# Kernel optimization log

Measured on AMD Instinct MI355X. Metric: run time of the kernel, lower is better.

Reference implementation:

```python
import jax, jax.numpy as jnp
import numpy as np

EMB_SIZE = 768
BLOCK_SIZE = 64
NUM_CLASS = 97
N = 4096
NUM_BLOCKS = EMB_SIZE // BLOCK_SIZE  # 12


def setup_inputs() -> dict:
    key = jax.random.key(0)
    k1, k2, k3 = jax.random.split(key, 3)
    head_embeddings = jax.random.normal(k1, (N, EMB_SIZE), dtype=jnp.float32)
    tail_embeddings = jax.random.normal(k2, (N, EMB_SIZE), dtype=jnp.float32)
    # xavier_uniform for [NUM_CLASS, EMB_SIZE*BLOCK_SIZE]
    fan_in = EMB_SIZE * BLOCK_SIZE
    fan_out = NUM_CLASS
    bound = float(np.sqrt(6.0 / (fan_in + fan_out)))
    W = jax.random.uniform(k3, (NUM_CLASS, EMB_SIZE * BLOCK_SIZE), dtype=jnp.float32,
                           minval=-bound, maxval=bound)
    b = jnp.full((NUM_CLASS,), 0.1, dtype=jnp.float32)
    return {"head_embeddings": head_embeddings, "tail_embeddings": tail_embeddings,
            "W": W, "b": b}


def reference(head_embeddings, tail_embeddings, W, b):
    n = head_embeddings.shape[0]
    b1 = head_embeddings.reshape(n, NUM_BLOCKS, BLOCK_SIZE)  # [N, K, S]
    b2 = tail_embeddings.reshape(n, NUM_BLOCKS, BLOCK_SIZE)  # [N, K, S]
    # block-wise outer product: [N, K, S, S] -> [N, K*S*S]
    bl = jnp.einsum('nki,nkj->nkij', b1, b2).reshape(n, EMB_SIZE * BLOCK_SIZE)
    logits = bl @ W.T + b  # [N, NUM_CLASS]
    return logits
```

## Files before the change

### kernel.cpp

```cpp
#include <hip/hip_runtime.h>
#include <hip/hip_bf16.h>
#include <stdint.h>

#define NROWS 4096
#define NCLS  97
#define EMB   768
#define KTOT  49152
#define OUT_ELEMS (NROWS * NCLS)
#define E_ELEMS  (NROWS * EMB)
#define NK32  (KTOT / 32)
#define WT_BYTES ((size_t)NK32 * 128 * 64)
#define EB_BYTES ((size_t)E_ELEMS * 2)

typedef __attribute__((ext_vector_type(8)))  short short8;
typedef __attribute__((ext_vector_type(4)))  float floatx4;
typedef __bf16 bf16x2 __attribute__((ext_vector_type(2)));
typedef __bf16 bf16x8 __attribute__((ext_vector_type(8)));

__device__ __forceinline__ uint32_t pkmul(uint32_t a, uint32_t b) {
  bf16x2 x = __builtin_bit_cast(bf16x2, a);
  bf16x2 y = __builtin_bit_cast(bf16x2, b);
  bf16x2 r = x * y;
  return __builtin_bit_cast(uint32_t, r);
}

__device__ __forceinline__ uint4 cvt8(float4 a, float4 b) {
  bf16x8 v;
  v[0] = (__bf16)a.x; v[1] = (__bf16)a.y; v[2] = (__bf16)a.z; v[3] = (__bf16)a.w;
  v[4] = (__bf16)b.x; v[5] = (__bf16)b.y; v[6] = (__bf16)b.z; v[7] = (__bf16)b.w;
  return __builtin_bit_cast(uint4, v);
}

__global__ void prep(const float* __restrict__ W,
                     const float* __restrict__ b1,
                     const float* __restrict__ b2,
                     uint4* __restrict__ wt,
                     uint4* __restrict__ b1b,
                     uint4* __restrict__ b2b,
                     int nmax)
{
  const int nwt = NK32 * 128 * 4;
  const int nE8 = E_ELEMS / 8;
  int t = blockIdx.x * blockDim.x + threadIdx.x;
  if (t >= nmax) return;
  if (t < nwt) {
    int eo = t & 3;
    int c  = (t >> 2) & 127;
    int kc = t >> 9;
    uint4 v = uint4{0u, 0u, 0u, 0u};
    if (c < NCLS) {
      const float4* p = (const float4*)(W + (size_t)c * KTOT + kc * 32 + eo * 8);
      v = cvt8(p[0], p[1]);
    }
    wt[t] = v;
  } else if (t < nwt + nE8) {
    int i = t - nwt;
    const float4* p = (const float4*)b1 + (size_t)2 * i;
    b1b[i] = cvt8(p[0], p[1]);
  } else {
    int i = t - nwt - nE8;
    const float4* p = (const float4*)b2 + (size_t)2 * i;
    b2b[i] = cvt8(p[0], p[1]);
  }
}

template<bool BMIR>
__global__ __launch_bounds__(256, 2)
void bilinear_main(const void* __restrict__ b1p,
                   const void* __restrict__ b2p,
                   const char* __restrict__ Wt,
                   const float* __restrict__ biasg,
                   float* __restrict__ P,
                   float* __restrict__ outd,
                   int klen)
{
  const int tid  = threadIdx.x;
  const int w    = tid >> 6;
  const int l    = tid & 63;
  const int l15  = l & 15;
  const int quad = l >> 4;
  const int mhalf = w & 1;
  const int chalf = w >> 1;
  const int bm = blockIdx.y;
  const int k0 = blockIdx.x * klen;

  int nrow[4];
#pragma unroll
  for (int rt = 0; rt < 4; ++rt) nrow[rt] = bm * 128 + mhalf * 64 + rt * 16 + l15;

  const char* wtl = Wt + (size_t)(k0 >> 5) * 8192
                       + (chalf * 64 + l15) * 64 + quad * 16;

  floatx4 acc[4][4];
#pragma unroll
  for (int rt = 0; rt < 4; ++rt)
#pragma unroll
    for (int ct = 0; ct < 4; ++ct)
      acc[rt][ct] = floatx4{0.f, 0.f, 0.f, 0.f};

  uint4 b2c[4][2];
  uint4 b1c[4];
  int cur_k = -1;
  const int nwin = klen >> 6;

  for (int gwin = 0; gwin < nwin; gwin += 8) {
    const int kap0 = k0 + (gwin << 6);
    const int kblk = kap0 >> 12;
    const int i0   = (kap0 >> 6) & 63;
    if (kblk != cur_k) {
      cur_k = kblk;
#pragma unroll
      for (int rt = 0; rt < 4; ++rt)
#pragma unroll
        for (int kh = 0; kh < 2; ++kh) {
          if (BMIR) {
            b2c[rt][kh] = *(const uint4*)((const char*)b2p +
                            (size_t)nrow[rt] * 1536 + kblk * 128 + kh * 64 + quad * 16);
          } else {
            const float* p = (const float*)b2p + (size_t)nrow[rt] * EMB +
                             kblk * 64 + kh * 32 + quad * 8;
            b2c[rt][kh] = cvt8(((const float4*)p)[0], ((const float4*)p)[1]);
          }
        }
    }
#pragma unroll
    for (int rt = 0; rt < 4; ++rt) {
      if (BMIR) {
        b1c[rt] = *(const uint4*)((const char*)b1p +
                     (size_t)nrow[rt] * 1536 + kblk * 128 + i0 * 2);
      } else {
        const float* p = (const float*)b1p + (size_t)nrow[rt] * EMB + kblk * 64 + i0;
        b1c[rt] = cvt8(((const float4*)p)[0], ((const float4*)p)[1]);
      }
    }

#pragma unroll
    for (int ii = 0; ii < 8; ++ii) {
      const char* pw = wtl + (size_t)(gwin + ii) * 16384;

      uint32_t s2[4];
#pragma unroll
      for (int rt = 0; rt < 4; ++rt) {
        uint32_t d = (&b1c[rt].x)[ii >> 1];
        uint32_t h = (ii & 1) ? (d >> 16) : (d & 0xffffu);
        s2[rt] = h | (h << 16);
      }

#pragma unroll
      for (int kh = 0; kh < 2; ++kh) {
        short8 wf[4];
#pragma unroll
        for (int ct = 0; ct < 4; ++ct)
          wf[ct] = __builtin_bit_cast(short8,
                     *(const uint4*)(pw + kh * 8192 + ct * 1024));
        uint4 afr[4];
#pragma unroll
        for (int rt = 0; rt < 4; ++rt) {
          afr[rt].x = pkmul(s2[rt], b2c[rt][kh].x);
          afr[rt].y = pkmul(s2[rt], b2c[rt][kh].y);
          afr[rt].z = pkmul(s2[rt], b2c[rt][kh].z);
          afr[rt].w = pkmul(s2[rt], b2c[rt][kh].w);
        }
#pragma unroll
        for (int rt = 0; rt < 4; ++rt) {
          short8 af = __builtin_bit_cast(short8, afr[rt]);
#pragma unroll
          for (int ct = 0; ct < 4; ++ct)
            acc[rt][ct] = __builtin_amdgcn_mfma_f32_16x16x32_bf16(
                              af, wf[ct], acc[rt][ct], 0, 0, 0);
        }
      }
    }
  }

  if (P) {
    float* Pb = P + (size_t)blockIdx.x * OUT_ELEMS;
#pragma unroll
    for (int rt = 0; rt < 4; ++rt)
#pragma unroll
      for (int ct = 0; ct < 4; ++ct) {
        const int c = chalf * 64 + ct * 16 + l15;
        if (c < NCLS) {
#pragma unroll
          for (int r = 0; r < 4; ++r) {
            const int row = bm * 128 + mhalf * 64 + rt * 16 + quad * 4 + r;
            Pb[(size_t)row * NCLS + c] = acc[rt][ct][r];
          }
        }
      }
  } else {
#pragma unroll
    for (int rt = 0; rt < 4; ++rt)
#pragma unroll
      for (int ct = 0; ct < 4; ++ct) {
        const int c = chalf * 64 + ct * 16 + l15;
        if (c < NCLS) {
          const float bv = biasg[c];
#pragma unroll
          for (int r = 0; r < 4; ++r) {
            const int row = bm * 128 + mhalf * 64 + rt * 16 + quad * 4 + r;
            outd[(size_t)row * NCLS + c] = acc[rt][ct][r] + bv;
          }
        }
      }
  }
}

__global__ void reduce_bias(const float* __restrict__ P,
                            const float* __restrict__ biasg,
                            float* __restrict__ out, int KS)
{
  int i = blockIdx.x * blockDim.x + threadIdx.x;
  const int n4 = OUT_ELEMS / 4;
  if (i >= n4) return;
  int c0 = (i * 4) % NCLS;
  int c1 = c0 + 1 == NCLS ? 0 : c0 + 1;
  int c2 = c1 + 1 == NCLS ? 0 : c1 + 1;
  int c3 = c2 + 1 == NCLS ? 0 : c2 + 1;
  float4 s;
  s.x = biasg[c0]; s.y = biasg[c1]; s.z = biasg[c2]; s.w = biasg[c3];
  const float4* P4 = (const float4*)P;
  for (int t = 0; t < KS; ++t) {
    float4 v = P4[(size_t)t * n4 + i];
    s.x += v.x; s.y += v.y; s.z += v.z; s.w += v.w;
  }
  ((float4*)out)[i] = s;
}

extern "C" void kernel_launch(void* const* d_in, const int* in_sizes, int n_in,
                              void* d_out, int out_size, void* d_ws, size_t ws_size,
                              hipStream_t stream) {
  const float* b1f = (const float*)d_in[0];
  const float* b2f = (const float*)d_in[1];
  const float* Wf  = (const float*)d_in[2];
  const float* bbf = (const float*)d_in[3];
  float* out = (float*)d_out;

  const size_t resv_full = WT_BYTES + 2 * EB_BYTES;
  const size_t slice     = (size_t)OUT_ELEMS * 4;
  static const int cands[] = {16, 12, 8, 6, 4, 3, 2, 1};

  int KS = 0; bool bmir = false;
  for (int i = 0; i < 8; ++i)
    if (resv_full + (size_t)cands[i] * slice <= ws_size) { KS = cands[i]; bmir = true; break; }
  if (!bmir)
    for (int i = 0; i < 8; ++i)
      if (WT_BYTES + (size_t)cands[i] * slice <= ws_size) { KS = cands[i]; break; }

  uint4* Wt  = (uint4*)d_ws;
  uint4* b1b = (uint4*)((char*)d_ws + WT_BYTES);
  uint4* b2b = (uint4*)((char*)d_ws + WT_BYTES + EB_BYTES);
  const int nwt = NK32 * 128 * 4;
  const int nE8 = E_ELEMS / 8;
  const int nprep = bmir ? (nwt + 2 * nE8) : nwt;

  prep<<<(nprep + 255) / 256, 256, 0, stream>>>(Wf, b1f, b2f, Wt, b1b, b2b, nprep);

  if (KS > 0) {
    float* P = (float*)((char*)d_ws + (bmir ? resv_full : WT_BYTES));
    if (bmir)
      bilinear_main<true><<<dim3(KS, 32), 256, 0, stream>>>(
          (const void*)b1b, (const void*)b2b, (const char*)Wt, bbf, P, nullptr, KTOT / KS);
    else
      bilinear_main<false><<<dim3(KS, 32), 256, 0, stream>>>(
          (const void*)b1f, (const void*)b2f, (const char*)Wt, bbf, P, nullptr, KTOT / KS);
    reduce_bias<<<(OUT_ELEMS / 4 + 255) / 256, 256, 0, stream>>>(P, bbf, out, KS);
  } else {
    bilinear_main<false><<<dim3(1, 32), 256, 0, stream>>>(
        (const void*)b1f, (const void*)b2f, (const char*)Wt, bbf, nullptr, out, KTOT);
  }
}
```

Baseline: 152.9 us.

## Skip padded class tile MFMAs, raise split-K factor, template reduce

```diff
diff --git a/kernel.cpp b/kernel.cpp
--- a/kernel.cpp
+++ b/kernel.cpp
@@ -81,6 +81,7 @@
   const int quad = l >> 4;
   const int mhalf = w & 1;
   const int chalf = w >> 1;
+  const bool cfull = (chalf == 0);
   const int bm = blockIdx.y;
   const int k0 = blockIdx.x * klen;
 
@@ -151,8 +152,9 @@
         short8 wf[4];
 #pragma unroll
         for (int ct = 0; ct < 4; ++ct)
-          wf[ct] = __builtin_bit_cast(short8,
-                     *(const uint4*)(pw + kh * 8192 + ct * 1024));
+          if (ct < 3 || cfull)
+            wf[ct] = __builtin_bit_cast(short8,
+                       *(const uint4*)(pw + kh * 8192 + ct * 1024));
         uint4 afr[4];
 #pragma unroll
         for (int rt = 0; rt < 4; ++rt) {
@@ -166,8 +168,9 @@
           short8 af = __builtin_bit_cast(short8, afr[rt]);
 #pragma unroll
           for (int ct = 0; ct < 4; ++ct)
-            acc[rt][ct] = __builtin_amdgcn_mfma_f32_16x16x32_bf16(
-                              af, wf[ct], acc[rt][ct], 0, 0, 0);
+            if (ct < 3 || cfull)
+              acc[rt][ct] = __builtin_amdgcn_mfma_f32_16x16x32_bf16(
+                                af, wf[ct], acc[rt][ct], 0, 0, 0);
         }
       }
     }
@@ -206,9 +209,10 @@
   }
 }
 
-__global__ void reduce_bias(const float* __restrict__ P,
-                            const float* __restrict__ biasg,
-                            float* __restrict__ out, int KS)
+template<int KSC>
+__global__ void reduce_bias_t(const float* __restrict__ P,
+                              const float* __restrict__ biasg,
+                              float* __restrict__ out)
 {
   int i = blockIdx.x * blockDim.x + threadIdx.x;
   const int n4 = OUT_ELEMS / 4;
@@ -220,11 +224,29 @@
   float4 s;
   s.x = biasg[c0]; s.y = biasg[c1]; s.z = biasg[c2]; s.w = biasg[c3];
   const float4* P4 = (const float4*)P;
-  for (int t = 0; t < KS; ++t) {
+#pragma unroll
+  for (int t = 0; t < KSC; ++t) {
     float4 v = P4[(size_t)t * n4 + i];
     s.x += v.x; s.y += v.y; s.z += v.z; s.w += v.w;
   }
   ((float4*)out)[i] = s;
+}
+
+static void launch_reduce(int KS, const float* P, const float* bb, float* out,
+                          hipStream_t stream) {
+  const int nb = (OUT_ELEMS / 4 + 255) / 256;
+  switch (KS) {
+    case 32: reduce_bias_t<32><<<nb, 256, 0, stream>>>(P, bb, out); break;
+    case 24: reduce_bias_t<24><<<nb, 256, 0, stream>>>(P, bb, out); break;
+    case 16: reduce_bias_t<16><<<nb, 256, 0, stream>>>(P, bb, out); break;
+    case 12: reduce_bias_t<12><<<nb, 256, 0, stream>>>(P, bb, out); break;
+    case 8:  reduce_bias_t<8><<<nb, 256, 0, stream>>>(P, bb, out);  break;
+    case 6:  reduce_bias_t<6><<<nb, 256, 0, stream>>>(P, bb, out);  break;
+    case 4:  reduce_bias_t<4><<<nb, 256, 0, stream>>>(P, bb, out);  break;
+    case 3:  reduce_bias_t<3><<<nb, 256, 0, stream>>>(P, bb, out);  break;
+    case 2:  reduce_bias_t<2><<<nb, 256, 0, stream>>>(P, bb, out);  break;
+    default: reduce_bias_t<1><<<nb, 256, 0, stream>>>(P, bb, out);  break;
+  }
 }
 
 extern "C" void kernel_launch(void* const* d_in, const int* in_sizes, int n_in,
@@ -238,13 +260,14 @@
 
   const size_t resv_full = WT_BYTES + 2 * EB_BYTES;
   const size_t slice     = (size_t)OUT_ELEMS * 4;
-  static const int cands[] = {16, 12, 8, 6, 4, 3, 2, 1};
+  static const int cands[] = {32, 24, 16, 12, 8, 6, 4, 3, 2, 1};
+  const int NC = 10;
 
   int KS = 0; bool bmir = false;
-  for (int i = 0; i < 8; ++i)
+  for (int i = 0; i < NC; ++i)
     if (resv_full + (size_t)cands[i] * slice <= ws_size) { KS = cands[i]; bmir = true; break; }
   if (!bmir)
-    for (int i = 0; i < 8; ++i)
+    for (int i = 0; i < NC; ++i)
       if (WT_BYTES + (size_t)cands[i] * slice <= ws_size) { KS = cands[i]; break; }
 
   uint4* Wt  = (uint4*)d_ws;
@@ -264,7 +287,7 @@
     else
       bilinear_main<false><<<dim3(KS, 32), 256, 0, stream>>>(
           (const void*)b1f, (const void*)b2f, (const char*)Wt, bbf, P, nullptr, KTOT / KS);
-    reduce_bias<<<(OUT_ELEMS / 4 + 255) / 256, 256, 0, stream>>>(P, bbf, out, KS);
+    launch_reduce(KS, P, bbf, out, stream);
   } else {
     bilinear_main<false><<<dim3(1, 32), 256, 0, stream>>>(
         (const void*)b1f, (const void*)b2f, (const char*)Wt, bbf, nullptr, out, KTOT);
```

Result: slower. 160.7 us (+5.1%).
